# Kernel optimization log

Hardware: AMD Instinct MI355X
Metric: run time of the kernel (lower is better)

## Reference

```python
import jax, jax.numpy as jnp
import numpy as np

EPS = 1e-12  # matches torch F.normalize eps and utils.get_diagonal threshold


def _geteig(feats, K):
    # feats: [B, C, H, W]
    B, C, H, W = feats.shape
    nH, nW = H // 4, W // 4
    # bilinear, align_corners=False (half-pixel centers) == jax.image.resize 'bilinear'
    f = jax.image.resize(feats, (B, C, nH, nW), method='bilinear')
    f = f.reshape(B, C, nH * nW).transpose(0, 2, 1)  # [B, N, C]
    norm = jnp.linalg.norm(f, axis=-1, keepdims=True)
    f = f / jnp.maximum(norm, EPS)  # L2-normalize per pixel

    def per_sample(x):  # x: [N, C]
        Wm = x @ x.T                       # cosine similarity [N, N]
        Wm = Wm * (Wm > 0)                 # keep positive affinities
        Wm = Wm / Wm.max()
        Wm = jax.lax.stop_gradient(Wm)     # original detaches before eigsh
        d = Wm.sum(axis=1)                 # degree (row sums), as in utils.get_diagonal
        d = jnp.where(d < EPS, 1.0, d)
        inv_sqrt = 1.0 / jnp.sqrt(d)
        L = jnp.diag(d) - Wm               # unnormalized Laplacian
        # generalized problem L v = lam D v  <=>  eigh of D^-1/2 L D^-1/2
        Ln = inv_sqrt[:, None] * L * inv_sqrt[None, :]
        Ln = 0.5 * (Ln + Ln.T)             # enforce symmetry for stability
        evals = jnp.linalg.eigh(Ln)[0]     # ascending
        return evals[:K]                   # K smallest (eigsh sigma=0, which='LM')

    return jax.vmap(per_sample)(f)  # [B, K]


def setup_inputs() -> dict:
    key = jax.random.key(0)
    feats = jax.random.normal(key, (8, 3, 160, 160), dtype=jnp.float32)
    return {"feats": feats, "K": 10}


def reference(feats, K):
    lan1 = _geteig(feats[:, :1], K)    # channel 0 -> [B, K]
    lan2 = _geteig(feats[:, 1:2], K)   # channel 1 -> [B, K]
    # NOTE: faithful to original bug: feats[:2:3] slices the BATCH dim -> [1, C, H, W]
    lan3 = _geteig(feats[:2:3], K)     # [1, K], broadcasts in the MSE below
    loss = jnp.mean((lan1 - lan2) ** 2)
    loss = loss + jnp.mean((lan1 - lan3) ** 2)
    loss = loss + jnp.mean((lan2 - lan3) ** 2)
    return loss * 5
```

## Files before the change

kernel.cpp:

```cpp
#include <hip/hip_runtime.h>
#include <math.h>

#define N16 1600
#define M 32
#define XSZ 51200
#define BIS_IT 28
#define EPSF 1e-12f


__device__ void taps1d(int o, int* lo, int* hi, float* wsum, float w[8]) {
  int l = 4 * o - 2, h = 4 * o + 5;
  if (l < 0) l = 0;
  if (h > 159) h = 159;
  float c = 4.f * o + 1.5f, s = 0.f;
  for (int x = l; x <= h; ++x) {
    float ww = 1.f - fabsf((float)x - c) * 0.25f;
    w[x - l] = ww;
    s += ww;
  }
  *lo = l; *hi = h; *wsum = s;
}

__global__ void __launch_bounds__(256)
k_resize(const float* __restrict__ in, float* __restrict__ rz) {
  const int bx = blockIdx.x, t = threadIdx.x;
  int map = bx / 7;
  int o = (bx % 7) * 256 + t;
  if (o >= N16) return;
  int oy = o / 40, ox = o % 40;
  int ly, hy, lx, hx; float sy, sx; float wy[8], wx[8];
  taps1d(oy, &ly, &hy, &sy, wy);
  taps1d(ox, &lx, &hx, &sx, wx);
  const float* src = in + (size_t)map * 160 * 160;
  float acc = 0.f;
  for (int y = ly; y <= hy; ++y) {
    float a = 0.f;
    const float* row = src + y * 160;
    for (int x = lx; x <= hx; ++x) a += wx[x - lx] * row[x];
    acc += wy[y - ly] * a;
  }
  rz[map * N16 + o] = acc / (sy * sx);
}

__global__ void __launch_bounds__(256)
k_prep(const float* __restrict__ rz, float* __restrict__ F,
       int* __restrict__ flags) {
  __shared__ int sp[256];
  __shared__ int sn[256];
  const int bx = blockIdx.x, t = threadIdx.x;
  if (bx < 16) {
    int b = bx >> 1, c = bx & 1;
    const float* m = rz + (b * 3 + c) * N16;
    int cp = 0, cn = 0;
    for (int o = t; o < N16; o += 256) {
      float v = m[o];
      cp += (v > 0.f);
      cn += (v < 0.f);
    }
    sp[t] = cp; sn[t] = cn;
    __syncthreads();
    for (int s = 128; s > 0; s >>= 1) {
      if (t < s) { sp[t] += sp[t + s]; sn[t] += sn[t + s]; }
      __syncthreads();
    }
    if (t == 0) flags[bx] = (sp[0] == 0 || sn[0] == 0) ? 1 : 0;
  } else {
    int n = (bx - 16) * 256 + t;
    if (n < N16) {
      float x = rz[n], y = rz[N16 + n], z = rz[2 * N16 + n];
      float nrm = sqrtf(x * x + y * y + z * z);
      float s = 1.f / fmaxf(nrm, EPSF);
      F[n * 3 + 0] = x * s;
      F[n * 3 + 1] = y * s;
      F[n * 3 + 2] = z * s;
    }
  }
}

__global__ void __launch_bounds__(256)
k_degree(const float* __restrict__ F, float* __restrict__ R,
         float* __restrict__ G4f, float* __restrict__ X0) {
  __shared__ float Fl[4800];
  __shared__ float red[256];
  const int bx = blockIdx.x, t = threadIdx.x;
  for (int s = t; s < 4800; s += 256) Fl[s] = F[s];
  __syncthreads();
  int rl = t >> 4, jt = t & 15;
  int i = bx * 16 + rl;
  float fx = Fl[i * 3], fy = Fl[i * 3 + 1], fz = Fl[i * 3 + 2];
  float s = 0.f;
#pragma unroll 8
  for (int j = jt; j < N16; j += 16) {
    float w = fx * Fl[j * 3] + fy * Fl[j * 3 + 1] + fz * Fl[j * 3 + 2];
    if (w > 0.f) s += w;
  }
  red[t] = s;
  __syncthreads();
  for (int st = 8; st > 0; st >>= 1) {
    if (jt < st) red[t] += red[t + st];
    __syncthreads();
  }
  if (jt == 0) {
    float d = red[t];
    if (d < EPSF) d = 1.f;
    float r = rsqrtf(d);
    R[i] = r;
    G4f[i * 4 + 0] = r * fx;
    G4f[i * 4 + 1] = r * fy;
    G4f[i * 4 + 2] = r * fz;
    G4f[i * 4 + 3] = 0.f;
  }
  for (int e = t; e < 512; e += 256) {
    int n = bx * 16 + (e >> 5);
    int k = e & 31;
    unsigned u = ((unsigned)n * 2654435761u) ^ ((unsigned)k * 0x9E3779B9u);
    u = u * 1664525u + 1013904223u;
    u ^= u >> 16; u *= 2246822519u; u ^= u >> 13;
    X0[n * M + k] = ((float)(u >> 8) * (1.f / 8388608.f)) - 1.f;
  }
}

__global__ void __launch_bounds__(256)
k_mv(const float* __restrict__ F, const float4* __restrict__ G4,
     const float* __restrict__ R, const float* __restrict__ Xin,
     float* __restrict__ Xout) {
  __shared__ float Ws[2][8 * 324];
  __shared__ float XsT[2][16 * 324];
  __shared__ float Red[16 * 136];
  const int bx = blockIdx.x, t = threadIdx.x;
  const int ig = bx >> 1, kh = bx & 1;
  const int i0 = ig * 8, kbase = kh * 16;
  const int rg = t & 3, kg = (t >> 2) & 3, jg = t >> 4;
  const int sj = t >> 2, sq = t & 3;
  const int wil = t & 7, wjg = t >> 3;
  const float fx = F[(i0 + wil) * 3 + 0];
  const float fy = F[(i0 + wil) * 3 + 1];
  const float fz = F[(i0 + wil) * 3 + 2];
  const float4* Xin4 = (const float4*)Xin;

  float acc[2][4];
#pragma unroll
  for (int r = 0; r < 2; ++r)
#pragma unroll
    for (int kk = 0; kk < 4; ++kk) acc[r][kk] = 0.f;

#pragma unroll
  for (int p = 0; p < 5; ++p) {
    float4 xs = Xin4[(size_t)(p * 64 + sj) * 8 + kh * 4 + sq];
    XsT[0][(sq * 4 + 0) * 324 + p * 64 + sj] = xs.x;
    XsT[0][(sq * 4 + 1) * 324 + p * 64 + sj] = xs.y;
    XsT[0][(sq * 4 + 2) * 324 + p * 64 + sj] = xs.z;
    XsT[0][(sq * 4 + 3) * 324 + p * 64 + sj] = xs.w;
  }
#pragma unroll
  for (int q = 0; q < 10; ++q) {
    float4 g = G4[wjg + 32 * q];
    Ws[0][wil * 324 + wjg + 32 * q] =
        fmaxf(fx * g.x + fy * g.y + fz * g.z, 0.f);
  }
  __syncthreads();

  for (int c = 0; c < 5; ++c) {
    const int cur = c & 1, nxt = cur ^ 1;
    float4 xsr[5];
    float4 gar[10];
    if (c < 4) {
      const int jb = (c + 1) * 320;
#pragma unroll
      for (int p = 0; p < 5; ++p)
        xsr[p] = Xin4[(size_t)(jb + p * 64 + sj) * 8 + kh * 4 + sq];
#pragma unroll
      for (int q = 0; q < 10; ++q) gar[q] = G4[jb + wjg + 32 * q];
    }
#pragma unroll
    for (int ss = 0; ss < 5; ++ss) {
      const int jq = ss * 64 + jg * 4;
      float4 wv[2], xv[4];
#pragma unroll
      for (int r = 0; r < 2; ++r)
        wv[r] = *(const float4*)&Ws[cur][(rg * 2 + r) * 324 + jq];
#pragma unroll
      for (int kk = 0; kk < 4; ++kk)
        xv[kk] = *(const float4*)&XsT[cur][(kg * 4 + kk) * 324 + jq];
#pragma unroll
      for (int r = 0; r < 2; ++r)
#pragma unroll
        for (int kk = 0; kk < 4; ++kk)
          acc[r][kk] += wv[r].x * xv[kk].x + wv[r].y * xv[kk].y +
                        wv[r].z * xv[kk].z + wv[r].w * xv[kk].w;
    }
    if (c < 4) {
#pragma unroll
      for (int p = 0; p < 5; ++p) {
        XsT[nxt][(sq * 4 + 0) * 324 + p * 64 + sj] = xsr[p].x;
        XsT[nxt][(sq * 4 + 1) * 324 + p * 64 + sj] = xsr[p].y;
        XsT[nxt][(sq * 4 + 2) * 324 + p * 64 + sj] = xsr[p].z;
        XsT[nxt][(sq * 4 + 3) * 324 + p * 64 + sj] = xsr[p].w;
      }
#pragma unroll
      for (int q = 0; q < 10; ++q)
        Ws[nxt][wil * 324 + wjg + 32 * q] =
            fmaxf(fx * gar[q].x + fy * gar[q].y + fz * gar[q].z, 0.f);
    }
    __syncthreads();
  }

#pragma unroll
  for (int r = 0; r < 2; ++r)
#pragma unroll
    for (int kk = 0; kk < 4; ++kk)
      Red[jg * 136 + (rg * 2 + r) * 16 + (kg * 4 + kk)] = acc[r][kk];
  __syncthreads();
  if (t < 128) {
    const int il = t >> 4, kl = t & 15;
    float sv = 0.f;
#pragma unroll
    for (int g = 0; g < 16; ++g) sv += Red[g * 136 + il * 16 + kl];
    const int gi = i0 + il, gk = kbase + kl;
    Xout[(size_t)gi * 32 + gk] =
        0.5f * Xin[(size_t)gi * 32 + gk] + 0.5f * R[gi] * sv;
  }
}

__global__ void __launch_bounds__(256)
k_gram(const float* __restrict__ Xa, const float* __restrict__ Xb,
       float* __restrict__ GPp) {
  __shared__ float sA[2048];
  __shared__ float sB[2048];
  const int bx = blockIdx.x, t = threadIdx.x;
  float acc[4] = {0.f, 0.f, 0.f, 0.f};
  for (int c = 0; c < 5; ++c) {
    const int j0 = bx * 320 + c * 64;
    __syncthreads();
    for (int s = t; s < 2048; s += 256) {
      sA[s] = Xa[(size_t)j0 * 32 + s];
      sB[s] = Xb[(size_t)j0 * 32 + s];
    }
    __syncthreads();
#pragma unroll
    for (int s = 0; s < 4; ++s) {
      int e = s * 256 + t;
      int a = e >> 5, b = e & 31;
      float sum = 0.f;
#pragma unroll 8
      for (int jl = 0; jl < 64; ++jl) sum += sA[jl * 32 + a] * sB[jl * 32 + b];
      acc[s] += sum;
    }
  }
#pragma unroll
  for (int s = 0; s < 4; ++s) GPp[(size_t)bx * 1024 + s * 256 + t] = acc[s];
}

__global__ void __launch_bounds__(256)
k_apply(const float* __restrict__ GPp, const float* __restrict__ Xin,
        float* __restrict__ Xout) {
  __shared__ float Gm[32 * 33];
  const int bx = blockIdx.x, t = threadIdx.x;
#pragma unroll
  for (int u = 0; u < 4; ++u) {
    int e = t + u * 256;
    float g = 0.f;
#pragma unroll
    for (int p = 0; p < 5; ++p) g += GPp[p * 1024 + e];
    Gm[(e >> 5) * 33 + (e & 31)] = g;
  }
  const int r = t >> 5, l = t & 31;
  const int row = bx * 8 + r;
  float x = Xin[(size_t)row * M + l];
  __syncthreads();
  if (t < 64) {
    for (int k = 0; k < 32; ++k) {
      if (t == k) Gm[k * 33 + k] = sqrtf(fmaxf(Gm[k * 33 + k], 1e-30f));
      float piv = Gm[k * 33 + k];
      if (t > k && t < 32) Gm[t * 33 + k] /= piv;
#pragma unroll
      for (int u = 0; u < 16; ++u) {
        int e = t + u * 64;
        int i = e >> 5, j = e & 31;
        if (i > k && j > k && j <= i)
          Gm[i * 33 + j] -= Gm[i * 33 + k] * Gm[j * 33 + k];
      }
    }
  }
  __syncthreads();
  const int half = t & 32;
  float y = 0.f;
  for (int k = 0; k < 32; ++k) {
    float gkl = Gm[k * 33 + l];
    float contrib = (l < k) ? y * gkl : 0.f;
#pragma unroll
    for (int o = 16; o; o >>= 1) contrib += __shfl_xor(contrib, o, 64);
    float xk = __shfl(x, half + k, 64);
    float yk = (xk - contrib) / Gm[k * 33 + k];
    if (l == k) y = yk;
  }
  Xout[(size_t)row * M + l] = y;
}

__device__ __forceinline__ float wred(float v) {
#pragma unroll
  for (int o = 32; o; o >>= 1) v += __shfl_xor(v, o, 64);
  return v;
}

__global__ void __launch_bounds__(64)
k_rr(const float* __restrict__ GPp, const int* __restrict__ flags,
     const int* __restrict__ Kptr, float* __restrict__ out) {
  __shared__ float Bs[1056];
  __shared__ float part[1024];
  __shared__ float evs[32];
  const int t = threadIdx.x;
#pragma unroll
  for (int u = 0; u < 16; ++u) {
    int e = t + u * 64;
    float g = 0.f;
#pragma unroll
    for (int p = 0; p < 5; ++p) g += GPp[p * 1024 + e];
    part[e] = g;
  }
  __syncthreads();
#pragma unroll
  for (int u = 0; u < 16; ++u) {
    int e = t + u * 64;
    int i = e >> 5, j = e & 31;
    Bs[i * 33 + j] = 0.5f * (part[e] + part[j * 32 + i]);
  }
  __syncthreads();
  const int tr = t & 31;
  float row[32];
#pragma unroll
  for (int c = 0; c < 32; ++c) row[c] = Bs[tr * 33 + c];
  float eer[32];
#pragma unroll
  for (int k = 0; k <= 29; ++k) {
    float xi = (t > k && t < 32) ? row[k] : 0.f;
    float nx2 = wred(xi * xi);
    float x0 = __shfl(xi, k + 1, 64);
    if (nx2 < 1e-28f) { eer[k] = x0; continue; }
    float alpha = (x0 >= 0.f) ? -sqrtf(nx2) : sqrtf(nx2);
    float h = nx2 - alpha * x0;
    float vv = (t == k + 1) ? (xi - alpha) : xi;
    eer[k] = alpha;
    float p0 = 0.f, p1 = 0.f, p2 = 0.f, p3 = 0.f;
#pragma unroll
    for (int c = 0; c < 32; c += 4) {
      p0 += row[c + 0] * __shfl(vv, c + 0, 64);
      p1 += row[c + 1] * __shfl(vv, c + 1, 64);
      p2 += row[c + 2] * __shfl(vv, c + 2, 64);
      p3 += row[c + 3] * __shfl(vv, c + 3, 64);
    }
    float pi = ((p0 + p1) + (p2 + p3)) / h;
    float vp = wred(vv * pi);
    float Kc = vp / (2.f * h);
    float uu = (t > k && t < 32) ? (pi - Kc * vv) : 0.f;
#pragma unroll
    for (int c = 0; c < 32; ++c) {
      float uc = __shfl(uu, c, 64);
      float vc = __shfl(vv, c, 64);
      row[c] -= vv * uc + uu * vc;
    }
  }
  float ddr[32];
#pragma unroll
  for (int c = 0; c < 32; ++c) ddr[c] = __shfl(row[c], c, 64);
  eer[30] = __shfl(row[30], 31, 64);
  eer[31] = 0.f;
  float ee2r[31];
#pragma unroll
  for (int c = 0; c < 31; ++c) ee2r[c] = eer[c] * eer[c];
  float lo = 1e30f, hi = -1e30f;
#pragma unroll
  for (int i = 0; i < 32; ++i) {
    float r = ((i > 0) ? fabsf(eer[i - 1]) : 0.f) +
              ((i < 31) ? fabsf(eer[i]) : 0.f);
    lo = fminf(lo, ddr[i] - r);
    hi = fmaxf(hi, ddr[i] + r);
  }
  lo -= 1e-6f; hi += 1e-6f;
  if (t < 32) {
    float a = lo, b = hi;
    for (int it = 0; it < BIS_IT; ++it) {
      float mid = 0.5f * (a + b);
      float q = ddr[0] - mid;
      int cnt = (q < 0.f) ? 1 : 0;
#pragma unroll
      for (int i = 1; i < 32; ++i) {
        float den = q;
        float ad = fabsf(den);
        den = (ad < 1e-30f) ? ((den < 0.f) ? -1e-30f : 1e-30f) : den;
        q = ddr[i] - mid - ee2r[i - 1] * __builtin_amdgcn_rcpf(den);
        cnt += (q < 0.f) ? 1 : 0;
      }
      if (cnt <= t) a = mid; else b = mid;
    }
    evs[t] = 0.5f * (a + b);
  }
  __syncthreads();
  if (t == 0) {
    int K = Kptr ? *Kptr : 10;
    if (K < 1) K = 10;
    if (K > 32) K = 32;
    float t12 = 0.f, t13 = 0.f, t23 = 0.f;
    for (int b = 0; b < 8; ++b) {
      float f1 = flags[b * 2 + 0] ? 1.f : 0.f;
      float f2 = flags[b * 2 + 1] ? 1.f : 0.f;
      for (int k = 0; k < K; ++k) {
        float v1 = (k == 0) ? 0.f : (k == 1 ? f1 : 1.f);
        float v2 = (k == 0) ? 0.f : (k == 1 ? f2 : 1.f);
        float m3 = 2.f - 2.f * evs[31 - k];
        t12 += (v1 - v2) * (v1 - v2);
        t13 += (v1 - m3) * (v1 - m3);
        t23 += (v2 - m3) * (v2 - m3);
      }
    }
    out[0] = 5.f * (t12 + t13 + t23) / (8.f * (float)K);
  }
}

extern "C" void kernel_launch(void* const* d_in, const int* in_sizes, int n_in,
                              void* d_out, int out_size, void* d_ws, size_t ws_size,
                              hipStream_t stream) {
  const float* feats = (const float*)d_in[0];
  const int* Kptr = (n_in > 1) ? (const int*)d_in[1] : nullptr;
  float* ws = (float*)d_ws;
  float* RZ = ws;
  float* F  = ws + 38400;
  float* G4f = ws + 43200;
  float* R  = ws + 49600;
  int* FLAGS = (int*)(ws + 51200);
  float* GP = ws + 51264;
  float* XB = ws + 51264 + 15360;
  float* bufs[4] = {XB, XB + XSZ, XB + 2 * XSZ, XB + 3 * XSZ};
  const float4* G4 = (const float4*)G4f;
  float* outp = (float*)d_out;

  k_resize<<<dim3(168), dim3(256), 0, stream>>>(feats, RZ);
  k_prep<<<dim3(23), dim3(256), 0, stream>>>(RZ, F, FLAGS);
  k_degree<<<dim3(100), dim3(256), 0, stream>>>(F, R, G4f, bufs[0]);

  const float* cur = bufs[0];
  for (int m = 1; m <= 10; ++m) {
    float* o = bufs[1 + m % 3];
    k_mv<<<dim3(400), dim3(256), 0, stream>>>(F, G4, R, cur, o);
    cur = o;
  }
  k_gram<<<dim3(5), dim3(256), 0, stream>>>(cur, cur, GP);
  k_apply<<<dim3(200), dim3(256), 0, stream>>>(GP, cur, bufs[0]);
  cur = bufs[0];
  for (int m = 11; m <= 20; ++m) {
    float* o = bufs[1 + m % 3];
    k_mv<<<dim3(400), dim3(256), 0, stream>>>(F, G4, R, cur, o);
    cur = o;
  }
  k_gram<<<dim3(5), dim3(256), 0, stream>>>(cur, cur, GP + 5120);
  k_apply<<<dim3(200), dim3(256), 0, stream>>>(GP + 5120, cur, bufs[0]);
  k_mv<<<dim3(400), dim3(256), 0, stream>>>(F, G4, R, bufs[0], bufs[1]);
  k_gram<<<dim3(5), dim3(256), 0, stream>>>(bufs[0], bufs[1], GP + 10240);
  k_rr<<<dim3(1), dim3(64), 0, stream>>>(GP + 10240, FLAGS, Kptr, outp);
}
```

Baseline: 502.8 us.

## Keep a transposed copy of iterate and read it directly in matvec

Every writer of the iterate block (degree init, matvec, apply) now also writes a column-major copy, so the matvec can read X^T straight from global memory as float4 instead of staging and transposing it through shared memory. The whole 8x1600 affinity row block is computed once into shared memory, which removes the double-buffered chunk loop and its per-chunk barriers. The final loss loop in k_rr is unrolled with the flags and eigenvalue terms held in registers. In exchange each kernel issues extra strided, uncoalesced transposed stores, X is read from global/L2 every step, and the larger shared-memory tile (about 60 KB) may lower occupancy.

```diff
diff --git a/kernel.cpp b/kernel.cpp
--- a/kernel.cpp
+++ b/kernel.cpp
@@ -6,6 +6,7 @@
 #define XSZ 51200
 #define BIS_IT 28
 #define EPSF 1e-12f
+#define WSTRIDE 1604
 
 
 __device__ void taps1d(int o, int* lo, int* hi, float* wsum, float w[8]) {
@@ -79,7 +80,8 @@
 
 __global__ void __launch_bounds__(256)
 k_degree(const float* __restrict__ F, float* __restrict__ R,
-         float* __restrict__ G4f, float* __restrict__ X0) {
+         float* __restrict__ G4f, float* __restrict__ X0,
+         float* __restrict__ X0T) {
   __shared__ float Fl[4800];
   __shared__ float red[256];
   const int bx = blockIdx.x, t = threadIdx.x;
@@ -116,27 +118,35 @@
     unsigned u = ((unsigned)n * 2654435761u) ^ ((unsigned)k * 0x9E3779B9u);
     u = u * 1664525u + 1013904223u;
     u ^= u >> 16; u *= 2246822519u; u ^= u >> 13;
-    X0[n * M + k] = ((float)(u >> 8) * (1.f / 8388608.f)) - 1.f;
+    float v = ((float)(u >> 8) * (1.f / 8388608.f)) - 1.f;
+    X0[n * M + k] = v;
+    X0T[(size_t)k * N16 + n] = v;
   }
 }
 
 __global__ void __launch_bounds__(256)
 k_mv(const float* __restrict__ F, const float4* __restrict__ G4,
      const float* __restrict__ R, const float* __restrict__ Xin,
-     float* __restrict__ Xout) {
-  __shared__ float Ws[2][8 * 324];
-  __shared__ float XsT[2][16 * 324];
+     const float* __restrict__ XTin, float* __restrict__ Xout,
+     float* __restrict__ XTout) {
+  __shared__ float Ws[8 * WSTRIDE];
   __shared__ float Red[16 * 136];
   const int bx = blockIdx.x, t = threadIdx.x;
   const int ig = bx >> 1, kh = bx & 1;
   const int i0 = ig * 8, kbase = kh * 16;
   const int rg = t & 3, kg = (t >> 2) & 3, jg = t >> 4;
-  const int sj = t >> 2, sq = t & 3;
   const int wil = t & 7, wjg = t >> 3;
   const float fx = F[(i0 + wil) * 3 + 0];
   const float fy = F[(i0 + wil) * 3 + 1];
   const float fz = F[(i0 + wil) * 3 + 2];
-  const float4* Xin4 = (const float4*)Xin;
+
+#pragma unroll 5
+  for (int q = 0; q < 50; ++q) {
+    int j = wjg + 32 * q;
+    float4 g = G4[j];
+    Ws[wil * WSTRIDE + j] = fmaxf(fx * g.x + fy * g.y + fz * g.z, 0.f);
+  }
+  __syncthreads();
 
   float acc[2][4];
 #pragma unroll
@@ -144,67 +154,25 @@
 #pragma unroll
     for (int kk = 0; kk < 4; ++kk) acc[r][kk] = 0.f;
 
-#pragma unroll
-  for (int p = 0; p < 5; ++p) {
-    float4 xs = Xin4[(size_t)(p * 64 + sj) * 8 + kh * 4 + sq];
-    XsT[0][(sq * 4 + 0) * 324 + p * 64 + sj] = xs.x;
-    XsT[0][(sq * 4 + 1) * 324 + p * 64 + sj] = xs.y;
-    XsT[0][(sq * 4 + 2) * 324 + p * 64 + sj] = xs.z;
-    XsT[0][(sq * 4 + 3) * 324 + p * 64 + sj] = xs.w;
-  }
-#pragma unroll
-  for (int q = 0; q < 10; ++q) {
-    float4 g = G4[wjg + 32 * q];
-    Ws[0][wil * 324 + wjg + 32 * q] =
-        fmaxf(fx * g.x + fy * g.y + fz * g.z, 0.f);
-  }
-  __syncthreads();
-
-  for (int c = 0; c < 5; ++c) {
-    const int cur = c & 1, nxt = cur ^ 1;
-    float4 xsr[5];
-    float4 gar[10];
-    if (c < 4) {
-      const int jb = (c + 1) * 320;
-#pragma unroll
-      for (int p = 0; p < 5; ++p)
-        xsr[p] = Xin4[(size_t)(jb + p * 64 + sj) * 8 + kh * 4 + sq];
-#pragma unroll
-      for (int q = 0; q < 10; ++q) gar[q] = G4[jb + wjg + 32 * q];
-    }
-#pragma unroll
-    for (int ss = 0; ss < 5; ++ss) {
-      const int jq = ss * 64 + jg * 4;
-      float4 wv[2], xv[4];
-#pragma unroll
-      for (int r = 0; r < 2; ++r)
-        wv[r] = *(const float4*)&Ws[cur][(rg * 2 + r) * 324 + jq];
+#pragma unroll 5
+  for (int cs = 0; cs < 25; ++cs) {
+    const int jq = cs * 64 + jg * 4;
+    float4 wv[2], xv[4];
+#pragma unroll
+    for (int kk = 0; kk < 4; ++kk)
+      xv[kk] = *(const float4*)&XTin[(size_t)(kbase + kg * 4 + kk) * N16 + jq];
+#pragma unroll
+    for (int r = 0; r < 2; ++r)
+      wv[r] = *(const float4*)&Ws[(rg * 2 + r) * WSTRIDE + jq];
+#pragma unroll
+    for (int r = 0; r < 2; ++r)
 #pragma unroll
       for (int kk = 0; kk < 4; ++kk)
-        xv[kk] = *(const float4*)&XsT[cur][(kg * 4 + kk) * 324 + jq];
-#pragma unroll
-      for (int r = 0; r < 2; ++r)
-#pragma unroll
-        for (int kk = 0; kk < 4; ++kk)
-          acc[r][kk] += wv[r].x * xv[kk].x + wv[r].y * xv[kk].y +
-                        wv[r].z * xv[kk].z + wv[r].w * xv[kk].w;
-    }
-    if (c < 4) {
-#pragma unroll
-      for (int p = 0; p < 5; ++p) {
-        XsT[nxt][(sq * 4 + 0) * 324 + p * 64 + sj] = xsr[p].x;
-        XsT[nxt][(sq * 4 + 1) * 324 + p * 64 + sj] = xsr[p].y;
-        XsT[nxt][(sq * 4 + 2) * 324 + p * 64 + sj] = xsr[p].z;
-        XsT[nxt][(sq * 4 + 3) * 324 + p * 64 + sj] = xsr[p].w;
-      }
-#pragma unroll
-      for (int q = 0; q < 10; ++q)
-        Ws[nxt][wil * 324 + wjg + 32 * q] =
-            fmaxf(fx * gar[q].x + fy * gar[q].y + fz * gar[q].z, 0.f);
-    }
-    __syncthreads();
-  }
-
+        acc[r][kk] += wv[r].x * xv[kk].x + wv[r].y * xv[kk].y +
+                      wv[r].z * xv[kk].z + wv[r].w * xv[kk].w;
+  }
+
+  __syncthreads();
 #pragma unroll
   for (int r = 0; r < 2; ++r)
 #pragma unroll
@@ -217,8 +185,9 @@
 #pragma unroll
     for (int g = 0; g < 16; ++g) sv += Red[g * 136 + il * 16 + kl];
     const int gi = i0 + il, gk = kbase + kl;
-    Xout[(size_t)gi * 32 + gk] =
-        0.5f * Xin[(size_t)gi * 32 + gk] + 0.5f * R[gi] * sv;
+    float v = 0.5f * Xin[(size_t)gi * 32 + gk] + 0.5f * R[gi] * sv;
+    Xout[(size_t)gi * 32 + gk] = v;
+    XTout[(size_t)gk * N16 + gi] = v;
   }
 }
 
@@ -253,7 +222,7 @@
 
 __global__ void __launch_bounds__(256)
 k_apply(const float* __restrict__ GPp, const float* __restrict__ Xin,
-        float* __restrict__ Xout) {
+        float* __restrict__ Xout, float* __restrict__ XTout) {
   __shared__ float Gm[32 * 33];
   const int bx = blockIdx.x, t = threadIdx.x;
 #pragma unroll
@@ -295,6 +264,7 @@
     if (l == k) y = yk;
   }
   Xout[(size_t)row * M + l] = y;
+  XTout[(size_t)l * N16 + row] = y;
 }
 
 __device__ __forceinline__ float wred(float v) {
@@ -400,17 +370,27 @@
     int K = Kptr ? *Kptr : 10;
     if (K < 1) K = 10;
     if (K > 32) K = 32;
+    float m3r[32];
+#pragma unroll
+    for (int k = 0; k < 32; ++k) m3r[k] = 2.f - 2.f * evs[31 - k];
+    int flr[16];
+#pragma unroll
+    for (int b = 0; b < 16; ++b) flr[b] = flags[b];
     float t12 = 0.f, t13 = 0.f, t23 = 0.f;
+#pragma unroll
     for (int b = 0; b < 8; ++b) {
-      float f1 = flags[b * 2 + 0] ? 1.f : 0.f;
-      float f2 = flags[b * 2 + 1] ? 1.f : 0.f;
-      for (int k = 0; k < K; ++k) {
-        float v1 = (k == 0) ? 0.f : (k == 1 ? f1 : 1.f);
-        float v2 = (k == 0) ? 0.f : (k == 1 ? f2 : 1.f);
-        float m3 = 2.f - 2.f * evs[31 - k];
-        t12 += (v1 - v2) * (v1 - v2);
-        t13 += (v1 - m3) * (v1 - m3);
-        t23 += (v2 - m3) * (v2 - m3);
+      float f1 = flr[b * 2 + 0] ? 1.f : 0.f;
+      float f2 = flr[b * 2 + 1] ? 1.f : 0.f;
+#pragma unroll
+      for (int k = 0; k < 32; ++k) {
+        if (k < K) {
+          float v1 = (k == 0) ? 0.f : (k == 1 ? f1 : 1.f);
+          float v2 = (k == 0) ? 0.f : (k == 1 ? f2 : 1.f);
+          float m3 = m3r[k];
+          t12 += (v1 - v2) * (v1 - v2);
+          t13 += (v1 - m3) * (v1 - m3);
+          t23 += (v2 - m3) * (v2 - m3);
+        }
       }
     }
     out[0] = 5.f * (t12 + t13 + t23) / (8.f * (float)K);
@@ -430,31 +410,37 @@
   int* FLAGS = (int*)(ws + 51200);
   float* GP = ws + 51264;
   float* XB = ws + 51264 + 15360;
+  float* XT = XB + 4 * XSZ;
   float* bufs[4] = {XB, XB + XSZ, XB + 2 * XSZ, XB + 3 * XSZ};
+  float* tbufs[4] = {XT, XT + XSZ, XT + 2 * XSZ, XT + 3 * XSZ};
   const float4* G4 = (const float4*)G4f;
   float* outp = (float*)d_out;
 
   k_resize<<<dim3(168), dim3(256), 0, stream>>>(feats, RZ);
   k_prep<<<dim3(23), dim3(256), 0, stream>>>(RZ, F, FLAGS);
-  k_degree<<<dim3(100), dim3(256), 0, stream>>>(F, R, G4f, bufs[0]);
-
-  const float* cur = bufs[0];
+  k_degree<<<dim3(100), dim3(256), 0, stream>>>(F, R, G4f, bufs[0], tbufs[0]);
+
+  int ci = 0;
   for (int m = 1; m <= 10; ++m) {
-    float* o = bufs[1 + m % 3];
-    k_mv<<<dim3(400), dim3(256), 0, stream>>>(F, G4, R, cur, o);
-    cur = o;
-  }
-  k_gram<<<dim3(5), dim3(256), 0, stream>>>(cur, cur, GP);
-  k_apply<<<dim3(200), dim3(256), 0, stream>>>(GP, cur, bufs[0]);
-  cur = bufs[0];
+    int oi = 1 + m % 3;
+    k_mv<<<dim3(400), dim3(256), 0, stream>>>(F, G4, R, bufs[ci], tbufs[ci],
+                                              bufs[oi], tbufs[oi]);
+    ci = oi;
+  }
+  k_gram<<<dim3(5), dim3(256), 0, stream>>>(bufs[ci], bufs[ci], GP);
+  k_apply<<<dim3(200), dim3(256), 0, stream>>>(GP, bufs[ci], bufs[0], tbufs[0]);
+  ci = 0;
   for (int m = 11; m <= 20; ++m) {
-    float* o = bufs[1 + m % 3];
-    k_mv<<<dim3(400), dim3(256), 0, stream>>>(F, G4, R, cur, o);
-    cur = o;
-  }
-  k_gram<<<dim3(5), dim3(256), 0, stream>>>(cur, cur, GP + 5120);
-  k_apply<<<dim3(200), dim3(256), 0, stream>>>(GP + 5120, cur, bufs[0]);
-  k_mv<<<dim3(400), dim3(256), 0, stream>>>(F, G4, R, bufs[0], bufs[1]);
+    int oi = 1 + m % 3;
+    k_mv<<<dim3(400), dim3(256), 0, stream>>>(F, G4, R, bufs[ci], tbufs[ci],
+                                              bufs[oi], tbufs[oi]);
+    ci = oi;
+  }
+  k_gram<<<dim3(5), dim3(256), 0, stream>>>(bufs[ci], bufs[ci], GP + 5120);
+  k_apply<<<dim3(200), dim3(256), 0, stream>>>(GP + 5120, bufs[ci], bufs[0],
+                                               tbufs[0]);
+  k_mv<<<dim3(400), dim3(256), 0, stream>>>(F, G4, R, bufs[0], tbufs[0],
+                                            bufs[1], tbufs[1]);
   k_gram<<<dim3(5), dim3(256), 0, stream>>>(bufs[0], bufs[1], GP + 10240);
   k_rr<<<dim3(1), dim3(64), 0, stream>>>(GP + 10240, FLAGS, Kptr, outp);
 }
```

New measurement: 711.2 us. +41.5%, slower.
